# Performance work log

Measured on AMD Instinct MI355X. Metric: run time of the kernel, lower is better.

The kernel has to match this reference:

```python
import jax, jax.numpy as jnp
import numpy as np

ALPHA = 0.2  # LeakyReLU negative slope

def setup_inputs() -> dict:
    key = jax.random.key(0)
    k_h, k_adj, k_W, k_a = jax.random.split(key, 4)
    B, N, F_in, F_out = 8, 2048, 256, 64
    h = jax.random.normal(k_h, (B, N, F_in), dtype=jnp.float32)
    adj = jax.random.randint(k_adj, (B, N, N), 0, 2, dtype=jnp.int32)
    # nn.Linear weights: W [F_out, F_in], a [1, 2*F_out]
    W = jax.random.normal(k_W, (F_out, F_in), dtype=jnp.float32) * (1.0 / np.sqrt(F_in))
    a = jax.random.normal(k_a, (1, 2 * F_out), dtype=jnp.float32) * (1.0 / np.sqrt(2 * F_out))
    return {"h": h, "adj": adj, "W": W, "a": a}

def reference(h, adj, W, a):
    # Wh = h @ W^T : [B, N, F_out]
    Wh = jnp.einsum('bnf,of->bno', h, W)
    F_out = Wh.shape[-1]
    # a([Wi, Wj]) decomposes: e_ij = a_i . Wh_i + a_j . Wh_j (no O(N^2 * 2F) concat)
    a_i = a[0, :F_out]   # [F_out]
    a_j = a[0, F_out:]   # [F_out]
    e_i = Wh @ a_i       # [B, N]
    e_j = Wh @ a_j       # [B, N]
    e = jax.nn.leaky_relu(e_i[:, :, None] + e_j[:, None, :], negative_slope=ALPHA)  # [B, N, N]
    e = jnp.where(adj == 0, -jnp.inf, e)
    att = jnp.nan_to_num(jax.nn.softmax(e, axis=-1), nan=0.0)
    # dropout is identity in eval mode
    return jnp.einsum('bnm,bmo->bno', att, Wh)
```

## Files before the change

### kernel.cpp

```cpp
#include <hip/hip_runtime.h>

typedef float f32x4 __attribute__((ext_vector_type(4)));
typedef __bf16 bf16x8 __attribute__((ext_vector_type(8)));
typedef int i32x4 __attribute__((ext_vector_type(4)));
typedef unsigned short u16;
typedef unsigned int u32;

#define ALPHA 0.2f

__device__ __forceinline__ u16 f2bf(float x) {
    u32 u = __float_as_uint(x);
    u += 0x7FFFu + ((u >> 16) & 1u);
    return (u16)(u >> 16);
}

__global__ __launch_bounds__(256) void k_wh(
    const float* __restrict__ hsrc, const float* __restrict__ Wsrc,
    const float* __restrict__ asrc,
    u16* __restrict__ WhbT,
    float* __restrict__ ei, float* __restrict__ ej)
{
    __shared__ float Wl[64][68];
    __shared__ float hl[64][68];
    __shared__ __align__(16) u16 tl[4096];

    const int tid = threadIdx.x;
    const int tx = tid & 15, ty = tid >> 4;
    const int R0 = blockIdx.x * 64;

    float acc[4][4] = {};

    for (int kc = 0; kc < 4; ++kc) {
        const int k0 = kc * 64;
        __syncthreads();
        #pragma unroll
        for (int p = 0; p < 4; ++p) {
            int idx = p * 1024 + tid * 4;
            int row = idx >> 6, k = idx & 63;
            float4 wv4 = *reinterpret_cast<const float4*>(&Wsrc[row * 256 + k0 + k]);
            Wl[k + 0][row] = wv4.x; Wl[k + 1][row] = wv4.y;
            Wl[k + 2][row] = wv4.z; Wl[k + 3][row] = wv4.w;
            float4 hv4 = *reinterpret_cast<const float4*>(&hsrc[(size_t)(R0 + row) * 256 + k0 + k]);
            hl[k + 0][row] = hv4.x; hl[k + 1][row] = hv4.y;
            hl[k + 2][row] = hv4.z; hl[k + 3][row] = hv4.w;
        }
        __syncthreads();
        #pragma unroll 4
        for (int k = 0; k < 64; ++k) {
            float4 hv = *reinterpret_cast<const float4*>(&hl[k][4 * ty]);
            float4 wv = *reinterpret_cast<const float4*>(&Wl[k][4 * tx]);
            float hr[4] = {hv.x, hv.y, hv.z, hv.w};
            float wc[4] = {wv.x, wv.y, wv.z, wv.w};
            #pragma unroll
            for (int i = 0; i < 4; ++i)
                #pragma unroll
                for (int j = 0; j < 4; ++j)
                    acc[i][j] = fmaf(hr[i], wc[j], acc[i][j]);
        }
    }

    float4 av_i = *reinterpret_cast<const float4*>(&asrc[4 * tx]);
    float4 av_j = *reinterpret_cast<const float4*>(&asrc[64 + 4 * tx]);
    #pragma unroll
    for (int i = 0; i < 4; ++i) {
        float pi = acc[i][0]*av_i.x + acc[i][1]*av_i.y + acc[i][2]*av_i.z + acc[i][3]*av_i.w;
        float pj = acc[i][0]*av_j.x + acc[i][1]*av_j.y + acc[i][2]*av_j.z + acc[i][3]*av_j.w;
        #pragma unroll
        for (int off = 1; off < 16; off <<= 1) {
            pi += __shfl_xor(pi, off, 64);
            pj += __shfl_xor(pj, off, 64);
        }
        if (tx == 0) {
            ei[R0 + 4 * ty + i] = pi;
            ej[R0 + 4 * ty + i] = pj;
        }
    }

    #pragma unroll
    for (int i = 0; i < 4; ++i)
        #pragma unroll
        for (int j = 0; j < 4; ++j) {
            int row = 4 * tx + j;
            int col = 4 * ty + i;
            tl[(row * 64 + col) ^ ((row & 7) << 3)] = f2bf(acc[i][j]);
        }
    __syncthreads();
    {
        const int b = blockIdx.x >> 5;
        const int nloc = (blockIdx.x & 31) * 64;
        const int o = tid >> 2, rg = tid & 3;
        #pragma unroll
        for (int c = 0; c < 2; ++c) {
            int u = (o * 64 + rg * 16 + 8 * c) ^ ((o & 7) << 3);
            int4 v = *reinterpret_cast<const int4*>(&tl[u]);
            *reinterpret_cast<int4*>(&WhbT[(size_t)(b * 64 + o) * 2048 + nloc + rg * 16 + 8 * c]) = v;
        }
    }
}

__global__ __launch_bounds__(256) void k_attn(
    const int* __restrict__ adj, const u16* __restrict__ WhbT,
    const float* __restrict__ ei_g, const float* __restrict__ ej_g,
    float* __restrict__ out)
{
    __shared__ float accl[2][64][21];

    const int tid   = threadIdx.x;
    const int lane  = tid & 63;
    const int wid   = tid >> 6;
    const int b     = blockIdx.x >> 6;
    const int blk   = blockIdx.x & 63;
    const int strip = wid & 1;
    const int half  = wid >> 1;
    const int n0    = blk * 32 + strip * 16;
    const int r     = lane & 15;
    const int ks    = lane >> 4;

    const int*   adjp = adj  + (size_t)(b * 2048 + n0 + r) * 2048 + half * 1024 + ks * 8;
    const float* ejp  = ej_g + b * 2048 + half * 1024 + ks * 8;
    const u16*   whp  = WhbT + (size_t)(b * 64 + r) * 2048 + half * 1024 + ks * 8;

    i32x4 Aa0, Aa1, Ba0, Ba1;
    float4 Ae0, Ae1, Be0, Be1;
    bf16x8 Aw0, Aw1, Aw2, Aw3, Bw0, Bw1, Bw2, Bw3;

#define LOADS(t, a0,a1,e0,e1,w0,w1,w2,w3) { \
    const int mo_ = (t) * 32; \
    a0 = *reinterpret_cast<const i32x4*>(adjp + mo_); \
    a1 = *reinterpret_cast<const i32x4*>(adjp + mo_ + 4); \
    e0 = *reinterpret_cast<const float4*>(ejp + mo_); \
    e1 = *reinterpret_cast<const float4*>(ejp + mo_ + 4); \
    w0 = *reinterpret_cast<const bf16x8*>(whp + mo_); \
    w1 = *reinterpret_cast<const bf16x8*>(whp + 32768 + mo_); \
    w2 = *reinterpret_cast<const bf16x8*>(whp + 65536 + mo_); \
    w3 = *reinterpret_cast<const bf16x8*>(whp + 98304 + mo_); }

    LOADS(0, Aa0,Aa1,Ae0,Ae1,Aw0,Aw1,Aw2,Aw3);
    LOADS(1, Ba0,Ba1,Be0,Be1,Bw0,Bw1,Bw2,Bw3);

    float mj = -1e30f;
    #pragma unroll
    for (int i = 0; i < 8; ++i) {
        float4 v = *reinterpret_cast<const float4*>(&ej_g[b * 2048 + (i * 64 + lane) * 4]);
        mj = fmaxf(mj, fmaxf(fmaxf(v.x, v.y), fmaxf(v.z, v.w)));
    }
    #pragma unroll
    for (int off = 1; off < 64; off <<= 1) mj = fmaxf(mj, __shfl_xor(mj, off, 64));

    const float eiv = ei_g[b * 2048 + n0 + r];
    const float xM  = eiv + mj;
    const float M   = fmaxf(xM, ALPHA * xM);

    bf16x8 bones;
    {
        const float o = (r == 0) ? 1.0f : 0.0f;
        #pragma unroll
        for (int j = 0; j < 8; ++j) bones[j] = (__bf16)o;
    }

    f32x4 acc0 = {}, acc1 = {}, acc2 = {}, acc3 = {}, acc4 = {};

#define PVAL(av, ev, dst) { \
    float e_ = eiv + (ev); \
    float lr_ = fmaxf(e_, ALPHA * e_); \
    float p_ = __expf(lr_ - M); \
    dst = (__bf16)(((av) != 0) ? p_ : 0.0f); }

#define PSTEP(a0,a1,e0,e1,w0,w1,w2,w3) { \
    bf16x8 af; \
    PVAL(a0.x, e0.x, af[0]); PVAL(a0.y, e0.y, af[1]); \
    PVAL(a0.z, e0.z, af[2]); PVAL(a0.w, e0.w, af[3]); \
    PVAL(a1.x, e1.x, af[4]); PVAL(a1.y, e1.y, af[5]); \
    PVAL(a1.z, e1.z, af[6]); PVAL(a1.w, e1.w, af[7]); \
    acc0 = __builtin_amdgcn_mfma_f32_16x16x32_bf16(af, w0, acc0, 0, 0, 0); \
    acc1 = __builtin_amdgcn_mfma_f32_16x16x32_bf16(af, w1, acc1, 0, 0, 0); \
    acc2 = __builtin_amdgcn_mfma_f32_16x16x32_bf16(af, w2, acc2, 0, 0, 0); \
    acc3 = __builtin_amdgcn_mfma_f32_16x16x32_bf16(af, w3, acc3, 0, 0, 0); \
    acc4 = __builtin_amdgcn_mfma_f32_16x16x32_bf16(af, bones, acc4, 0, 0, 0); }

    for (int k = 0; k < 15; ++k) {
        const int t = 2 * k;
        PSTEP(Aa0,Aa1,Ae0,Ae1,Aw0,Aw1,Aw2,Aw3);
        LOADS(t + 2, Aa0,Aa1,Ae0,Ae1,Aw0,Aw1,Aw2,Aw3);
        PSTEP(Ba0,Ba1,Be0,Be1,Bw0,Bw1,Bw2,Bw3);
        LOADS(t + 3, Ba0,Ba1,Be0,Be1,Bw0,Bw1,Bw2,Bw3);
    }
    PSTEP(Aa0,Aa1,Ae0,Ae1,Aw0,Aw1,Aw2,Aw3);
    PSTEP(Ba0,Ba1,Be0,Be1,Bw0,Bw1,Bw2,Bw3);

#undef LOADS
#undef PSTEP
#undef PVAL

    if (half == 1) {
        #pragma unroll
        for (int q = 0; q < 4; ++q) {
            accl[strip][lane][q]      = acc0[q];
            accl[strip][lane][4 + q]  = acc1[q];
            accl[strip][lane][8 + q]  = acc2[q];
            accl[strip][lane][12 + q] = acc3[q];
            accl[strip][lane][16 + q] = acc4[q];
        }
    }
    __syncthreads();
    if (half == 0) {
        #pragma unroll
        for (int q = 0; q < 4; ++q) {
            acc0[q] += accl[strip][lane][q];
            acc1[q] += accl[strip][lane][4 + q];
            acc2[q] += accl[strip][lane][8 + q];
            acc3[q] += accl[strip][lane][12 + q];
            acc4[q] += accl[strip][lane][16 + q];
        }
        #pragma unroll
        for (int q = 0; q < 4; ++q) {
            float d   = __shfl(acc4[q], lane & 48, 64);
            float inv = (d > 0.0f) ? 1.0f / d : 0.0f;
            const int n = n0 + ks * 4 + q;
            float* op = out + (size_t)(b * 2048 + n) * 64 + r;
            op[0]  = acc0[q] * inv;
            op[16] = acc1[q] * inv;
            op[32] = acc2[q] * inv;
            op[48] = acc3[q] * inv;
        }
    }
}

extern "C" void kernel_launch(void* const* d_in, const int* in_sizes, int n_in,
                              void* d_out, int out_size, void* d_ws, size_t ws_size,
                              hipStream_t stream)
{
    const float* h   = (const float*)d_in[0];
    const int*   adj = (const int*)d_in[1];
    const float* W   = (const float*)d_in[2];
    const float* a   = (const float*)d_in[3];
    float* out = (float*)d_out;

    u16*   WhbT = (u16*)d_ws;
    float* ei   = (float*)((char*)d_ws + 2 * 1024 * 1024);
    float* ej   = ei + 16384;

    k_wh<<<dim3(256), dim3(256), 0, stream>>>(h, W, a, WhbT, ei, ej);
    k_attn<<<dim3(512), dim3(256), 0, stream>>>(adj, WhbT, ei, ej, out);
}
```

Baseline: 69.93 us.

## Pack adjacency into bitmasks in the Wh kernel and split attention over four waves

Extra blocks in the first kernel read the int32 adjacency with nontemporal loads and pack it into 32-bit bitmasks laid out for the attention kernel. The attention kernel then loads one int4 of mask bits per lane instead of streaming the full adjacency row inside the MFMA loop. The column range is now split across four waves per 16-row strip (1024 blocks), and partial sums are reduced through shared memory. The dense adjacency is still read once, so the gain depends on taking that stream out of the compute loop and overlapping it with the Wh GEMM, at the cost of an extra workspace round trip.

```diff
diff --git a/kernel.cpp b/kernel.cpp
--- a/kernel.cpp
+++ b/kernel.cpp
@@ -7,6 +7,7 @@
 typedef unsigned int u32;
 
 #define ALPHA 0.2f
+#define NPACK 2048
 
 __device__ __forceinline__ u16 f2bf(float x) {
     u32 u = __float_as_uint(x);
@@ -14,17 +15,46 @@
     return (u16)(u >> 16);
 }
 
-__global__ __launch_bounds__(256) void k_wh(
+__global__ __launch_bounds__(256) void k_wh_pack(
     const float* __restrict__ hsrc, const float* __restrict__ Wsrc,
-    const float* __restrict__ asrc,
+    const float* __restrict__ asrc, const int* __restrict__ adj,
     u16* __restrict__ WhbT,
-    float* __restrict__ ei, float* __restrict__ ej)
+    float* __restrict__ ei, float* __restrict__ ej,
+    u32* __restrict__ adjq)
 {
     __shared__ float Wl[64][68];
     __shared__ float hl[64][68];
     __shared__ __align__(16) u16 tl[4096];
 
     const int tid = threadIdx.x;
+
+    if (blockIdx.x >= 256) {
+        int i = (blockIdx.x - 256) * 256 + tid;
+        #pragma unroll
+        for (int it = 0; it < 2; ++it, i += NPACK * 256) {
+            const int T = i & 3, ks = (i >> 2) & 3, q = (i >> 4) & 3;
+            const int row = i >> 6;
+            const int* base = adj + (size_t)row * 2048 + q * 512 + ks * 8;
+            u32 bits = 0;
+            #pragma unroll
+            for (int dt = 0; dt < 4; ++dt) {
+                const int c0 = (4 * T + dt) * 32;
+                i32x4 v0 = __builtin_nontemporal_load(
+                    reinterpret_cast<const i32x4*>(base + c0));
+                i32x4 v1 = __builtin_nontemporal_load(
+                    reinterpret_cast<const i32x4*>(base + c0 + 4));
+                u32 m = 0;
+                m |= (v0[0] != 0) ? 1u : 0u;  m |= (v0[1] != 0) ? 2u : 0u;
+                m |= (v0[2] != 0) ? 4u : 0u;  m |= (v0[3] != 0) ? 8u : 0u;
+                m |= (v1[0] != 0) ? 16u : 0u; m |= (v1[1] != 0) ? 32u : 0u;
+                m |= (v1[2] != 0) ? 64u : 0u; m |= (v1[3] != 0) ? 128u : 0u;
+                bits |= m << (dt * 8);
+            }
+            adjq[i] = bits;
+        }
+        return;
+    }
+
     const int tx = tid & 15, ty = tid >> 4;
     const int R0 = blockIdx.x * 64;
 
@@ -98,36 +128,52 @@
     }
 }
 
-__global__ __launch_bounds__(256) void k_attn(
-    const int* __restrict__ adj, const u16* __restrict__ WhbT,
+__global__ __launch_bounds__(256, 4) void k_attn(
+    const u32* __restrict__ adjq, const u16* __restrict__ WhbT,
     const float* __restrict__ ei_g, const float* __restrict__ ej_g,
     float* __restrict__ out)
 {
-    __shared__ float accl[2][64][21];
-
-    const int tid   = threadIdx.x;
-    const int lane  = tid & 63;
-    const int wid   = tid >> 6;
-    const int b     = blockIdx.x >> 6;
-    const int blk   = blockIdx.x & 63;
-    const int strip = wid & 1;
-    const int half  = wid >> 1;
-    const int n0    = blk * 32 + strip * 16;
-    const int r     = lane & 15;
-    const int ks    = lane >> 4;
-
-    const int*   adjp = adj  + (size_t)(b * 2048 + n0 + r) * 2048 + half * 1024 + ks * 8;
-    const float* ejp  = ej_g + b * 2048 + half * 1024 + ks * 8;
-    const u16*   whp  = WhbT + (size_t)(b * 64 + r) * 2048 + half * 1024 + ks * 8;
-
-    i32x4 Aa0, Aa1, Ba0, Ba1;
+    __shared__ float accl[3][64][21];
+
+    const int tid  = threadIdx.x;
+    const int lane = tid & 63;
+    const int mq   = tid >> 6;
+    const int b    = blockIdx.x >> 7;
+    const int n0   = (blockIdx.x & 127) * 16;
+    const int r    = lane & 15;
+    const int ks   = lane >> 4;
+
+    const float* ejp = ej_g + b * 2048 + mq * 512 + ks * 8;
+    const u16*   whp = WhbT + (size_t)(b * 64 + r) * 2048 + mq * 512 + ks * 8;
+
+    const i32x4 W4 = *reinterpret_cast<const i32x4*>(
+        &adjq[(size_t)(((b * 2048 + n0 + r) * 4 + mq) * 4 + ks) * 4]);
+
+    float mj = -1e30f;
+    #pragma unroll
+    for (int i = 0; i < 8; ++i) {
+        float4 v = *reinterpret_cast<const float4*>(&ej_g[b * 2048 + (i * 64 + lane) * 4]);
+        mj = fmaxf(mj, fmaxf(fmaxf(v.x, v.y), fmaxf(v.z, v.w)));
+    }
+    #pragma unroll
+    for (int off = 1; off < 64; off <<= 1) mj = fmaxf(mj, __shfl_xor(mj, off, 64));
+
+    const float eiv = ei_g[b * 2048 + n0 + r];
+    const float xM  = eiv + mj;
+    const float M   = fmaxf(xM, ALPHA * xM);
+
+    bf16x8 bones;
+    {
+        const float o = (r == 0) ? 1.0f : 0.0f;
+        #pragma unroll
+        for (int j = 0; j < 8; ++j) bones[j] = (__bf16)o;
+    }
+
+    f32x4 acc0 = {}, acc1 = {}, acc2 = {}, acc3 = {}, acc4 = {};
     float4 Ae0, Ae1, Be0, Be1;
     bf16x8 Aw0, Aw1, Aw2, Aw3, Bw0, Bw1, Bw2, Bw3;
 
-#define LOADS(t, a0,a1,e0,e1,w0,w1,w2,w3) { \
-    const int mo_ = (t) * 32; \
-    a0 = *reinterpret_cast<const i32x4*>(adjp + mo_); \
-    a1 = *reinterpret_cast<const i32x4*>(adjp + mo_ + 4); \
+#define LD(t, e0,e1,w0,w1,w2,w3) { const int mo_ = (t) * 32; \
     e0 = *reinterpret_cast<const float4*>(ejp + mo_); \
     e1 = *reinterpret_cast<const float4*>(ejp + mo_ + 4); \
     w0 = *reinterpret_cast<const bf16x8*>(whp + mo_); \
@@ -135,82 +181,62 @@
     w2 = *reinterpret_cast<const bf16x8*>(whp + 65536 + mo_); \
     w3 = *reinterpret_cast<const bf16x8*>(whp + 98304 + mo_); }
 
-    LOADS(0, Aa0,Aa1,Ae0,Ae1,Aw0,Aw1,Aw2,Aw3);
-    LOADS(1, Ba0,Ba1,Be0,Be1,Bw0,Bw1,Bw2,Bw3);
-
-    float mj = -1e30f;
-    #pragma unroll
-    for (int i = 0; i < 8; ++i) {
-        float4 v = *reinterpret_cast<const float4*>(&ej_g[b * 2048 + (i * 64 + lane) * 4]);
-        mj = fmaxf(mj, fmaxf(fmaxf(v.x, v.y), fmaxf(v.z, v.w)));
-    }
-    #pragma unroll
-    for (int off = 1; off < 64; off <<= 1) mj = fmaxf(mj, __shfl_xor(mj, off, 64));
-
-    const float eiv = ei_g[b * 2048 + n0 + r];
-    const float xM  = eiv + mj;
-    const float M   = fmaxf(xM, ALPHA * xM);
-
-    bf16x8 bones;
-    {
-        const float o = (r == 0) ? 1.0f : 0.0f;
-        #pragma unroll
-        for (int j = 0; j < 8; ++j) bones[j] = (__bf16)o;
-    }
-
-    f32x4 acc0 = {}, acc1 = {}, acc2 = {}, acc3 = {}, acc4 = {};
-
-#define PVAL(av, ev, dst) { \
+#define PVAL(mk, ev, dst) { \
     float e_ = eiv + (ev); \
     float lr_ = fmaxf(e_, ALPHA * e_); \
     float p_ = __expf(lr_ - M); \
-    dst = (__bf16)(((av) != 0) ? p_ : 0.0f); }
-
-#define PSTEP(a0,a1,e0,e1,w0,w1,w2,w3) { \
+    dst = (__bf16)((mk) ? p_ : 0.0f); }
+
+#define TILE(t, e0,e1,w0,w1,w2,w3) { \
+    const u32 byv = ((u32)W4[(t) >> 2]) >> (((t) & 3) * 8); \
     bf16x8 af; \
-    PVAL(a0.x, e0.x, af[0]); PVAL(a0.y, e0.y, af[1]); \
-    PVAL(a0.z, e0.z, af[2]); PVAL(a0.w, e0.w, af[3]); \
-    PVAL(a1.x, e1.x, af[4]); PVAL(a1.y, e1.y, af[5]); \
-    PVAL(a1.z, e1.z, af[6]); PVAL(a1.w, e1.w, af[7]); \
+    PVAL(byv & 1u,   e0.x, af[0]); PVAL(byv & 2u,   e0.y, af[1]); \
+    PVAL(byv & 4u,   e0.z, af[2]); PVAL(byv & 8u,   e0.w, af[3]); \
+    PVAL(byv & 16u,  e1.x, af[4]); PVAL(byv & 32u,  e1.y, af[5]); \
+    PVAL(byv & 64u,  e1.z, af[6]); PVAL(byv & 128u, e1.w, af[7]); \
     acc0 = __builtin_amdgcn_mfma_f32_16x16x32_bf16(af, w0, acc0, 0, 0, 0); \
     acc1 = __builtin_amdgcn_mfma_f32_16x16x32_bf16(af, w1, acc1, 0, 0, 0); \
     acc2 = __builtin_amdgcn_mfma_f32_16x16x32_bf16(af, w2, acc2, 0, 0, 0); \
     acc3 = __builtin_amdgcn_mfma_f32_16x16x32_bf16(af, w3, acc3, 0, 0, 0); \
     acc4 = __builtin_amdgcn_mfma_f32_16x16x32_bf16(af, bones, acc4, 0, 0, 0); }
 
-    for (int k = 0; k < 15; ++k) {
-        const int t = 2 * k;
-        PSTEP(Aa0,Aa1,Ae0,Ae1,Aw0,Aw1,Aw2,Aw3);
-        LOADS(t + 2, Aa0,Aa1,Ae0,Ae1,Aw0,Aw1,Aw2,Aw3);
-        PSTEP(Ba0,Ba1,Be0,Be1,Bw0,Bw1,Bw2,Bw3);
-        LOADS(t + 3, Ba0,Ba1,Be0,Be1,Bw0,Bw1,Bw2,Bw3);
-    }
-    PSTEP(Aa0,Aa1,Ae0,Ae1,Aw0,Aw1,Aw2,Aw3);
-    PSTEP(Ba0,Ba1,Be0,Be1,Bw0,Bw1,Bw2,Bw3);
-
-#undef LOADS
-#undef PSTEP
+#define PAIR(t) \
+    TILE(t,   Ae0,Ae1,Aw0,Aw1,Aw2,Aw3); LD((t)+2, Ae0,Ae1,Aw0,Aw1,Aw2,Aw3); \
+    TILE((t)+1, Be0,Be1,Bw0,Bw1,Bw2,Bw3); LD((t)+3, Be0,Be1,Bw0,Bw1,Bw2,Bw3);
+
+    LD(0, Ae0,Ae1,Aw0,Aw1,Aw2,Aw3);
+    LD(1, Be0,Be1,Bw0,Bw1,Bw2,Bw3);
+    PAIR(0); PAIR(2); PAIR(4); PAIR(6); PAIR(8); PAIR(10); PAIR(12);
+    TILE(14, Ae0,Ae1,Aw0,Aw1,Aw2,Aw3);
+    TILE(15, Be0,Be1,Bw0,Bw1,Bw2,Bw3);
+
+#undef PAIR
+#undef TILE
 #undef PVAL
-
-    if (half == 1) {
+#undef LD
+
+    if (mq != 0) {
         #pragma unroll
         for (int q = 0; q < 4; ++q) {
-            accl[strip][lane][q]      = acc0[q];
-            accl[strip][lane][4 + q]  = acc1[q];
-            accl[strip][lane][8 + q]  = acc2[q];
-            accl[strip][lane][12 + q] = acc3[q];
-            accl[strip][lane][16 + q] = acc4[q];
+            accl[mq - 1][lane][q]      = acc0[q];
+            accl[mq - 1][lane][4 + q]  = acc1[q];
+            accl[mq - 1][lane][8 + q]  = acc2[q];
+            accl[mq - 1][lane][12 + q] = acc3[q];
+            accl[mq - 1][lane][16 + q] = acc4[q];
         }
     }
     __syncthreads();
-    if (half == 0) {
-        #pragma unroll
-        for (int q = 0; q < 4; ++q) {
-            acc0[q] += accl[strip][lane][q];
-            acc1[q] += accl[strip][lane][4 + q];
-            acc2[q] += accl[strip][lane][8 + q];
-            acc3[q] += accl[strip][lane][12 + q];
-            acc4[q] += accl[strip][lane][16 + q];
+    if (mq == 0) {
+        #pragma unroll
+        for (int w = 0; w < 3; ++w) {
+            #pragma unroll
+            for (int q = 0; q < 4; ++q) {
+                acc0[q] += accl[w][lane][q];
+                acc1[q] += accl[w][lane][4 + q];
+                acc2[q] += accl[w][lane][8 + q];
+                acc3[q] += accl[w][lane][12 + q];
+                acc4[q] += accl[w][lane][16 + q];
+            }
         }
         #pragma unroll
         for (int q = 0; q < 4; ++q) {
@@ -239,7 +265,8 @@
     u16*   WhbT = (u16*)d_ws;
     float* ei   = (float*)((char*)d_ws + 2 * 1024 * 1024);
     float* ej   = ei + 16384;
-
-    k_wh<<<dim3(256), dim3(256), 0, stream>>>(h, W, a, WhbT, ei, ej);
-    k_attn<<<dim3(512), dim3(256), 0, stream>>>(adj, WhbT, ei, ej, out);
-}
+    u32*   adjq = (u32*)((char*)d_ws + 3 * 1024 * 1024);
+
+    k_wh_pack<<<dim3(256 + NPACK), dim3(256), 0, stream>>>(h, W, a, adj, WhbT, ei, ej, adjq);
+    k_attn<<<dim3(1024), dim3(256), 0, stream>>>(adjq, WhbT, ei, ej, out);
+}
```

Result: slower. 71.52 us (+2.3%).

## Stage Wh tiles in LDS, widen row tiles, split-K partials with normalize kernel

Applied to the files above, without the earlier changes.

The attention kernel now has each block handle 64 rows and one half of the key dimension. The bf16 Wh^T chunk and ej values are staged in shared memory and reused by all four waves, instead of each wave streaming Wh from global memory. Adjacency rows are read with nontemporal loads, four steps deep, and block indices are remapped so blocks are interleaved across batches. Partial numerators and denominators from the two halves go to workspace, and a third kernel sums and normalizes them. This adds a launch, extra global traffic for the partials, and barriers inside the main loop.

```diff
diff --git a/kernel.cpp b/kernel.cpp
--- a/kernel.cpp
+++ b/kernel.cpp
@@ -101,42 +101,42 @@
 __global__ __launch_bounds__(256) void k_attn(
     const int* __restrict__ adj, const u16* __restrict__ WhbT,
     const float* __restrict__ ei_g, const float* __restrict__ ej_g,
-    float* __restrict__ out)
-{
-    __shared__ float accl[2][64][21];
-
-    const int tid   = threadIdx.x;
-    const int lane  = tid & 63;
-    const int wid   = tid >> 6;
-    const int b     = blockIdx.x >> 6;
-    const int blk   = blockIdx.x & 63;
-    const int strip = wid & 1;
-    const int half  = wid >> 1;
-    const int n0    = blk * 32 + strip * 16;
-    const int r     = lane & 15;
-    const int ks    = lane >> 4;
-
-    const int*   adjp = adj  + (size_t)(b * 2048 + n0 + r) * 2048 + half * 1024 + ks * 8;
-    const float* ejp  = ej_g + b * 2048 + half * 1024 + ks * 8;
-    const u16*   whp  = WhbT + (size_t)(b * 64 + r) * 2048 + half * 1024 + ks * 8;
-
-    i32x4 Aa0, Aa1, Ba0, Ba1;
-    float4 Ae0, Ae1, Be0, Be1;
-    bf16x8 Aw0, Aw1, Aw2, Aw3, Bw0, Bw1, Bw2, Bw3;
-
-#define LOADS(t, a0,a1,e0,e1,w0,w1,w2,w3) { \
-    const int mo_ = (t) * 32; \
-    a0 = *reinterpret_cast<const i32x4*>(adjp + mo_); \
-    a1 = *reinterpret_cast<const i32x4*>(adjp + mo_ + 4); \
-    e0 = *reinterpret_cast<const float4*>(ejp + mo_); \
-    e1 = *reinterpret_cast<const float4*>(ejp + mo_ + 4); \
-    w0 = *reinterpret_cast<const bf16x8*>(whp + mo_); \
-    w1 = *reinterpret_cast<const bf16x8*>(whp + 32768 + mo_); \
-    w2 = *reinterpret_cast<const bf16x8*>(whp + 65536 + mo_); \
-    w3 = *reinterpret_cast<const bf16x8*>(whp + 98304 + mo_); }
-
-    LOADS(0, Aa0,Aa1,Ae0,Ae1,Aw0,Aw1,Aw2,Aw3);
-    LOADS(1, Ba0,Ba1,Be0,Be1,Bw0,Bw1,Bw2,Bw3);
+    float* __restrict__ nump, float* __restrict__ denp)
+{
+    __shared__ __align__(16) u16 whl[64 * 264];
+    __shared__ __align__(16) float ejl[1024];
+
+    const int tid  = threadIdx.x;
+    const int lane = tid & 63;
+    const int w    = tid >> 6;
+    const int lb = (blockIdx.x & 7) * 64 + (blockIdx.x >> 3);
+    const int mt = lb & 1;
+    const int nt = (lb >> 1) & 31;
+    const int b  = lb >> 6;
+    const int r  = lane & 15;
+    const int ks = lane >> 4;
+    const int m0 = mt * 1024;
+
+    {
+        float4 v = *reinterpret_cast<const float4*>(&ej_g[b * 2048 + m0 + tid * 4]);
+        *reinterpret_cast<float4*>(&ejl[tid * 4]) = v;
+    }
+
+    const u16* whb = WhbT + (size_t)b * 131072;
+    const int sf = tid >> 2;
+    const int su = (tid & 3) * 8;
+    int4 pv0, pv1, pv2, pv3, pv4, pv5, pv6, pv7;
+#define PLOAD(p) { const u16* pp = whb + sf * 2048 + m0 + (p) * 256 + su * 8; \
+    pv0 = *reinterpret_cast<const int4*>(pp);      pv1 = *reinterpret_cast<const int4*>(pp + 8); \
+    pv2 = *reinterpret_cast<const int4*>(pp + 16); pv3 = *reinterpret_cast<const int4*>(pp + 24); \
+    pv4 = *reinterpret_cast<const int4*>(pp + 32); pv5 = *reinterpret_cast<const int4*>(pp + 40); \
+    pv6 = *reinterpret_cast<const int4*>(pp + 48); pv7 = *reinterpret_cast<const int4*>(pp + 56); }
+#define PWRITE() { char* wp = reinterpret_cast<char*>(whl) + sf * 528 + su * 16; \
+    *reinterpret_cast<int4*>(wp)       = pv0; *reinterpret_cast<int4*>(wp + 16)  = pv1; \
+    *reinterpret_cast<int4*>(wp + 32)  = pv2; *reinterpret_cast<int4*>(wp + 48)  = pv3; \
+    *reinterpret_cast<int4*>(wp + 64)  = pv4; *reinterpret_cast<int4*>(wp + 80)  = pv5; \
+    *reinterpret_cast<int4*>(wp + 96)  = pv6; *reinterpret_cast<int4*>(wp + 112) = pv7; }
+    PLOAD(0);
 
     float mj = -1e30f;
     #pragma unroll
@@ -147,7 +147,7 @@
     #pragma unroll
     for (int off = 1; off < 64; off <<= 1) mj = fmaxf(mj, __shfl_xor(mj, off, 64));
 
-    const float eiv = ei_g[b * 2048 + n0 + r];
+    const float eiv = ei_g[b * 2048 + nt * 64 + w * 16 + r];
     const float xM  = eiv + mj;
     const float M   = fmaxf(xM, ALPHA * xM);
 
@@ -158,72 +158,98 @@
         for (int j = 0; j < 8; ++j) bones[j] = (__bf16)o;
     }
 
+    const int* adjp = adj + (size_t)(b * 2048 + nt * 64 + w * 16 + r) * 2048 + m0 + ks * 8;
+
+    i32x4 Aa0, Aa1, Ba0, Ba1, Ca0, Ca1, Da0, Da1;
+#define LADJ(gt, x0, x1) if ((gt) < 32) { \
+    x0 = __builtin_nontemporal_load(reinterpret_cast<const i32x4*>(adjp + (gt) * 32)); \
+    x1 = __builtin_nontemporal_load(reinterpret_cast<const i32x4*>(adjp + (gt) * 32 + 4)); }
+    LADJ(0, Aa0, Aa1); LADJ(1, Ba0, Ba1); LADJ(2, Ca0, Ca1); LADJ(3, Da0, Da1);
+
+    PWRITE();
+    __syncthreads();
+
     f32x4 acc0 = {}, acc1 = {}, acc2 = {}, acc3 = {}, acc4 = {};
 
-#define PVAL(av, ev, dst) { \
+    const char* wl0 = reinterpret_cast<const char*>(whl) + r * 528 + ks * 16;
+    const float* eb = ejl + ks * 8;
+
+#define PVAL(mk, ev, dst) { \
     float e_ = eiv + (ev); \
     float lr_ = fmaxf(e_, ALPHA * e_); \
     float p_ = __expf(lr_ - M); \
-    dst = (__bf16)(((av) != 0) ? p_ : 0.0f); }
-
-#define PSTEP(a0,a1,e0,e1,w0,w1,w2,w3) { \
+    dst = (__bf16)(((mk) != 0) ? p_ : 0.0f); }
+
+#define STEP(gt, x0, x1) { \
+    const int tl_ = (gt) & 7; \
+    float4 e0 = *reinterpret_cast<const float4*>(eb + (gt) * 32); \
+    float4 e1 = *reinterpret_cast<const float4*>(eb + (gt) * 32 + 4); \
     bf16x8 af; \
-    PVAL(a0.x, e0.x, af[0]); PVAL(a0.y, e0.y, af[1]); \
-    PVAL(a0.z, e0.z, af[2]); PVAL(a0.w, e0.w, af[3]); \
-    PVAL(a1.x, e1.x, af[4]); PVAL(a1.y, e1.y, af[5]); \
-    PVAL(a1.z, e1.z, af[6]); PVAL(a1.w, e1.w, af[7]); \
+    PVAL(x0[0], e0.x, af[0]); PVAL(x0[1], e0.y, af[1]); \
+    PVAL(x0[2], e0.z, af[2]); PVAL(x0[3], e0.w, af[3]); \
+    PVAL(x1[0], e1.x, af[4]); PVAL(x1[1], e1.y, af[5]); \
+    PVAL(x1[2], e1.z, af[6]); PVAL(x1[3], e1.w, af[7]); \
+    bf16x8 w0 = *reinterpret_cast<const bf16x8*>(wl0 + tl_ * 64); \
+    bf16x8 w1 = *reinterpret_cast<const bf16x8*>(wl0 + tl_ * 64 + 16 * 528); \
+    bf16x8 w2 = *reinterpret_cast<const bf16x8*>(wl0 + tl_ * 64 + 32 * 528); \
+    bf16x8 w3 = *reinterpret_cast<const bf16x8*>(wl0 + tl_ * 64 + 48 * 528); \
     acc0 = __builtin_amdgcn_mfma_f32_16x16x32_bf16(af, w0, acc0, 0, 0, 0); \
     acc1 = __builtin_amdgcn_mfma_f32_16x16x32_bf16(af, w1, acc1, 0, 0, 0); \
     acc2 = __builtin_amdgcn_mfma_f32_16x16x32_bf16(af, w2, acc2, 0, 0, 0); \
     acc3 = __builtin_amdgcn_mfma_f32_16x16x32_bf16(af, w3, acc3, 0, 0, 0); \
     acc4 = __builtin_amdgcn_mfma_f32_16x16x32_bf16(af, bones, acc4, 0, 0, 0); }
 
-    for (int k = 0; k < 15; ++k) {
-        const int t = 2 * k;
-        PSTEP(Aa0,Aa1,Ae0,Ae1,Aw0,Aw1,Aw2,Aw3);
-        LOADS(t + 2, Aa0,Aa1,Ae0,Ae1,Aw0,Aw1,Aw2,Aw3);
-        PSTEP(Ba0,Ba1,Be0,Be1,Bw0,Bw1,Bw2,Bw3);
-        LOADS(t + 3, Ba0,Ba1,Be0,Be1,Bw0,Bw1,Bw2,Bw3);
-    }
-    PSTEP(Aa0,Aa1,Ae0,Ae1,Aw0,Aw1,Aw2,Aw3);
-    PSTEP(Ba0,Ba1,Be0,Be1,Bw0,Bw1,Bw2,Bw3);
-
-#undef LOADS
-#undef PSTEP
+    #pragma unroll
+    for (int p = 0; p < 4; ++p) {
+        if (p < 3) PLOAD(p + 1);
+        STEP(p * 8 + 0, Aa0, Aa1); LADJ(p * 8 + 4,  Aa0, Aa1);
+        STEP(p * 8 + 1, Ba0, Ba1); LADJ(p * 8 + 5,  Ba0, Ba1);
+        STEP(p * 8 + 2, Ca0, Ca1); LADJ(p * 8 + 6,  Ca0, Ca1);
+        STEP(p * 8 + 3, Da0, Da1); LADJ(p * 8 + 7,  Da0, Da1);
+        STEP(p * 8 + 4, Aa0, Aa1); LADJ(p * 8 + 8,  Aa0, Aa1);
+        STEP(p * 8 + 5, Ba0, Ba1); LADJ(p * 8 + 9,  Ba0, Ba1);
+        STEP(p * 8 + 6, Ca0, Ca1); LADJ(p * 8 + 10, Ca0, Ca1);
+        STEP(p * 8 + 7, Da0, Da1); LADJ(p * 8 + 11, Da0, Da1);
+        if (p < 3) {
+            __syncthreads();
+            PWRITE();
+            __syncthreads();
+        }
+    }
+#undef STEP
 #undef PVAL
-
-    if (half == 1) {
-        #pragma unroll
-        for (int q = 0; q < 4; ++q) {
-            accl[strip][lane][q]      = acc0[q];
-            accl[strip][lane][4 + q]  = acc1[q];
-            accl[strip][lane][8 + q]  = acc2[q];
-            accl[strip][lane][12 + q] = acc3[q];
-            accl[strip][lane][16 + q] = acc4[q];
-        }
-    }
-    __syncthreads();
-    if (half == 0) {
-        #pragma unroll
-        for (int q = 0; q < 4; ++q) {
-            acc0[q] += accl[strip][lane][q];
-            acc1[q] += accl[strip][lane][4 + q];
-            acc2[q] += accl[strip][lane][8 + q];
-            acc3[q] += accl[strip][lane][12 + q];
-            acc4[q] += accl[strip][lane][16 + q];
-        }
-        #pragma unroll
-        for (int q = 0; q < 4; ++q) {
-            float d   = __shfl(acc4[q], lane & 48, 64);
-            float inv = (d > 0.0f) ? 1.0f / d : 0.0f;
-            const int n = n0 + ks * 4 + q;
-            float* op = out + (size_t)(b * 2048 + n) * 64 + r;
-            op[0]  = acc0[q] * inv;
-            op[16] = acc1[q] * inv;
-            op[32] = acc2[q] * inv;
-            op[48] = acc3[q] * inv;
-        }
-    }
+#undef LADJ
+#undef PWRITE
+#undef PLOAD
+
+    const size_t nb0 = (size_t)mt * 16384 + b * 2048 + nt * 64 + w * 16;
+    #pragma unroll
+    for (int q = 0; q < 4; ++q) {
+        const int rr = ks * 4 + q;
+        float* np = nump + (nb0 + rr) * 64 + r;
+        np[0]  = acc0[q];
+        np[16] = acc1[q];
+        np[32] = acc2[q];
+        np[48] = acc3[q];
+        if (r == 0) denp[nb0 + rr] = acc4[q];
+    }
+}
+
+__global__ __launch_bounds__(256) void k_norm(
+    const float* __restrict__ nump, const float* __restrict__ denp,
+    float* __restrict__ out)
+{
+    const int tid = threadIdx.x;
+    const int f4 = tid & 15;
+    const size_t N = (size_t)blockIdx.x * 16 + (tid >> 4);
+    const float d = denp[N] + denp[16384 + N];
+    const float inv = (d > 0.0f) ? 1.0f / d : 0.0f;
+    float4 a = *reinterpret_cast<const float4*>(&nump[N * 64 + f4 * 4]);
+    float4 c = *reinterpret_cast<const float4*>(&nump[(16384 + N) * 64 + f4 * 4]);
+    float4 o;
+    o.x = (a.x + c.x) * inv; o.y = (a.y + c.y) * inv;
+    o.z = (a.z + c.z) * inv; o.w = (a.w + c.w) * inv;
+    *reinterpret_cast<float4*>(&out[N * 64 + f4 * 4]) = o;
 }
 
 extern "C" void kernel_launch(void* const* d_in, const int* in_sizes, int n_in,
@@ -239,7 +265,10 @@
     u16*   WhbT = (u16*)d_ws;
     float* ei   = (float*)((char*)d_ws + 2 * 1024 * 1024);
     float* ej   = ei + 16384;
-
-    k_wh<<<dim3(256), dim3(256), 0, stream>>>(h, W, a, WhbT, ei, ej);
-    k_attn<<<dim3(512), dim3(256), 0, stream>>>(adj, WhbT, ei, ej, out);
-}
+    float* nump = (float*)((char*)d_ws + 4 * 1024 * 1024);
+    float* denp = (float*)((char*)d_ws + 12 * 1024 * 1024);
+
+    k_wh  <<<dim3(256),  dim3(256), 0, stream>>>(h, W, a, WhbT, ei, ej);
+    k_attn<<<dim3(512),  dim3(256), 0, stream>>>(adj, WhbT, ei, ej, nump, denp);
+    k_norm<<<dim3(1024), dim3(256), 0, stream>>>(nump, denp, out);
+}
```

Result: faster. 64.91 us (-7.2%).

## Prefetch whole adjacency slice into bitmasks and split attention K four ways

Applied to the files above, without the earlier changes.

Each wave now issues all sixteen of its adjacency vector loads up front as nontemporal loads and packs them into 32-bit masks. This puts many more bytes in flight for the bandwidth-bound int32 adjacency stream. Blocks now cover 16 rows with four waves each owning a quarter of the columns, and partial results are combined through shared memory. The grid doubles to 1024 blocks and is remapped so the eight consecutive block IDs go to different batches. The ej values are staged in LDS pre-scaled by log2(e), so the softmax numerator can use exp2f. The cost is higher register pressure from the 32 live adjacency vectors, which the launch bound of 4 blocks per CU may force into spills, plus a larger cross-wave reduction.

```diff
diff --git a/kernel.cpp b/kernel.cpp
--- a/kernel.cpp
+++ b/kernel.cpp
@@ -7,6 +7,7 @@
 typedef unsigned int u32;
 
 #define ALPHA 0.2f
+#define LOG2E 1.4426950408889634f
 
 __device__ __forceinline__ u16 f2bf(float x) {
     u32 u = __float_as_uint(x);
@@ -98,45 +99,22 @@
     }
 }
 
-__global__ __launch_bounds__(256) void k_attn(
+__global__ __launch_bounds__(256, 4) void k_attn(
     const int* __restrict__ adj, const u16* __restrict__ WhbT,
     const float* __restrict__ ei_g, const float* __restrict__ ej_g,
     float* __restrict__ out)
 {
-    __shared__ float accl[2][64][21];
-
-    const int tid   = threadIdx.x;
-    const int lane  = tid & 63;
-    const int wid   = tid >> 6;
-    const int b     = blockIdx.x >> 6;
-    const int blk   = blockIdx.x & 63;
-    const int strip = wid & 1;
-    const int half  = wid >> 1;
-    const int n0    = blk * 32 + strip * 16;
-    const int r     = lane & 15;
-    const int ks    = lane >> 4;
-
-    const int*   adjp = adj  + (size_t)(b * 2048 + n0 + r) * 2048 + half * 1024 + ks * 8;
-    const float* ejp  = ej_g + b * 2048 + half * 1024 + ks * 8;
-    const u16*   whp  = WhbT + (size_t)(b * 64 + r) * 2048 + half * 1024 + ks * 8;
-
-    i32x4 Aa0, Aa1, Ba0, Ba1;
-    float4 Ae0, Ae1, Be0, Be1;
-    bf16x8 Aw0, Aw1, Aw2, Aw3, Bw0, Bw1, Bw2, Bw3;
-
-#define LOADS(t, a0,a1,e0,e1,w0,w1,w2,w3) { \
-    const int mo_ = (t) * 32; \
-    a0 = *reinterpret_cast<const i32x4*>(adjp + mo_); \
-    a1 = *reinterpret_cast<const i32x4*>(adjp + mo_ + 4); \
-    e0 = *reinterpret_cast<const float4*>(ejp + mo_); \
-    e1 = *reinterpret_cast<const float4*>(ejp + mo_ + 4); \
-    w0 = *reinterpret_cast<const bf16x8*>(whp + mo_); \
-    w1 = *reinterpret_cast<const bf16x8*>(whp + 32768 + mo_); \
-    w2 = *reinterpret_cast<const bf16x8*>(whp + 65536 + mo_); \
-    w3 = *reinterpret_cast<const bf16x8*>(whp + 98304 + mo_); }
-
-    LOADS(0, Aa0,Aa1,Ae0,Ae1,Aw0,Aw1,Aw2,Aw3);
-    LOADS(1, Ba0,Ba1,Be0,Be1,Bw0,Bw1,Bw2,Bw3);
+    __shared__ float ejl[4][520];
+    __shared__ float comb[3][64][21];
+
+    const int tid  = threadIdx.x;
+    const int lane = tid & 63;
+    const int mq   = tid >> 6;
+    const int lb   = (int)(blockIdx.x & 7) * 128 + (int)(blockIdx.x >> 3);
+    const int b    = lb >> 7;
+    const int n0   = (lb & 127) * 16;
+    const int r    = lane & 15;
+    const int ks   = lane >> 4;
 
     float mj = -1e30f;
     #pragma unroll
@@ -147,9 +125,55 @@
     #pragma unroll
     for (int off = 1; off < 64; off <<= 1) mj = fmaxf(mj, __shfl_xor(mj, off, 64));
 
-    const float eiv = ei_g[b * 2048 + n0 + r];
-    const float xM  = eiv + mj;
-    const float M   = fmaxf(xM, ALPHA * xM);
+    const float eiv2 = ei_g[b * 2048 + n0 + r] * LOG2E;
+    const float xM2  = eiv2 + mj * LOG2E;
+    const float M2   = fmaxf(xM2, ALPHA * xM2);
+
+    {
+        float4 v0 = *reinterpret_cast<const float4*>(&ej_g[b * 2048 + mq * 512 + lane * 8]);
+        float4 v1 = *reinterpret_cast<const float4*>(&ej_g[b * 2048 + mq * 512 + lane * 8 + 4]);
+        v0.x *= LOG2E; v0.y *= LOG2E; v0.z *= LOG2E; v0.w *= LOG2E;
+        v1.x *= LOG2E; v1.y *= LOG2E; v1.z *= LOG2E; v1.w *= LOG2E;
+        *reinterpret_cast<float4*>(&ejl[mq][lane * 8])     = v0;
+        *reinterpret_cast<float4*>(&ejl[mq][lane * 8 + 4]) = v1;
+    }
+
+    const int* adjp = adj + (size_t)(b * 2048 + n0 + r) * 2048 + mq * 512 + ks * 8;
+    u32 bits0 = 0, bits1 = 0, bits2 = 0, bits3 = 0;
+    i32x4 Aq0, Aq1, Bq0, Bq1, Cq0, Cq1, Dq0, Dq1;
+    i32x4 Eq0, Eq1, Fq0, Fq1, Gq0, Gq1, Hq0, Hq1;
+
+#define LA(t, x0, x1) { \
+    x0 = __builtin_nontemporal_load(reinterpret_cast<const i32x4*>(adjp + (t) * 32)); \
+    x1 = __builtin_nontemporal_load(reinterpret_cast<const i32x4*>(adjp + (t) * 32 + 4)); }
+#define PK(x0, x1, W, sh) { u32 m_ = 0; \
+    m_ |= (x0[0] != 0) ? 1u   : 0u; m_ |= (x0[1] != 0) ? 2u   : 0u; \
+    m_ |= (x0[2] != 0) ? 4u   : 0u; m_ |= (x0[3] != 0) ? 8u   : 0u; \
+    m_ |= (x1[0] != 0) ? 16u  : 0u; m_ |= (x1[1] != 0) ? 32u  : 0u; \
+    m_ |= (x1[2] != 0) ? 64u  : 0u; m_ |= (x1[3] != 0) ? 128u : 0u; \
+    W |= m_ << (sh); }
+
+    LA(0, Aq0, Aq1); LA(1, Bq0, Bq1); LA(2, Cq0, Cq1); LA(3, Dq0, Dq1);
+    LA(4, Eq0, Eq1); LA(5, Fq0, Fq1); LA(6, Gq0, Gq1); LA(7, Hq0, Hq1);
+
+    PK(Aq0, Aq1, bits0, 0);  LA(8,  Aq0, Aq1);
+    PK(Bq0, Bq1, bits0, 8);  LA(9,  Bq0, Bq1);
+    PK(Cq0, Cq1, bits0, 16); LA(10, Cq0, Cq1);
+    PK(Dq0, Dq1, bits0, 24); LA(11, Dq0, Dq1);
+    PK(Eq0, Eq1, bits1, 0);  LA(12, Eq0, Eq1);
+    PK(Fq0, Fq1, bits1, 8);  LA(13, Fq0, Fq1);
+    PK(Gq0, Gq1, bits1, 16); LA(14, Gq0, Gq1);
+    PK(Hq0, Hq1, bits1, 24); LA(15, Hq0, Hq1);
+    PK(Aq0, Aq1, bits2, 0);
+    PK(Bq0, Bq1, bits2, 8);
+    PK(Cq0, Cq1, bits2, 16);
+    PK(Dq0, Dq1, bits2, 24);
+    PK(Eq0, Eq1, bits3, 0);
+    PK(Fq0, Fq1, bits3, 8);
+    PK(Gq0, Gq1, bits3, 16);
+    PK(Hq0, Hq1, bits3, 24);
+#undef PK
+#undef LA
 
     bf16x8 bones;
     {
@@ -158,59 +182,83 @@
         for (int j = 0; j < 8; ++j) bones[j] = (__bf16)o;
     }
 
+    const u16*   whp = WhbT + (size_t)(b * 64 + r) * 2048 + mq * 512 + ks * 8;
+    const float* eb  = &ejl[mq][ks * 8];
+
+    bf16x8 Aw0, Aw1, Aw2, Aw3, Bw0, Bw1, Bw2, Bw3;
+#define LDW(t, w0, w1, w2, w3) { const u16* pp = whp + (t) * 32; \
+    w0 = *reinterpret_cast<const bf16x8*>(pp); \
+    w1 = *reinterpret_cast<const bf16x8*>(pp + 32768); \
+    w2 = *reinterpret_cast<const bf16x8*>(pp + 65536); \
+    w3 = *reinterpret_cast<const bf16x8*>(pp + 98304); }
+
+#define PVAL(mk, ev, dst) { \
+    float x_ = eiv2 + (ev); \
+    float lr_ = fmaxf(x_, ALPHA * x_); \
+    float p_ = exp2f(lr_ - M2); \
+    dst = (__bf16)(((mk) != 0u) ? p_ : 0.0f); }
+
     f32x4 acc0 = {}, acc1 = {}, acc2 = {}, acc3 = {}, acc4 = {};
 
-#define PVAL(av, ev, dst) { \
-    float e_ = eiv + (ev); \
-    float lr_ = fmaxf(e_, ALPHA * e_); \
-    float p_ = __expf(lr_ - M); \
-    dst = (__bf16)(((av) != 0) ? p_ : 0.0f); }
-
-#define PSTEP(a0,a1,e0,e1,w0,w1,w2,w3) { \
+#define STEP(t, BW, w0, w1, w2, w3) { \
+    const u32 by_ = (BW) >> (((t) & 3) * 8); \
+    float4 e0 = *reinterpret_cast<const float4*>(eb + (t) * 32); \
+    float4 e1 = *reinterpret_cast<const float4*>(eb + (t) * 32 + 4); \
     bf16x8 af; \
-    PVAL(a0.x, e0.x, af[0]); PVAL(a0.y, e0.y, af[1]); \
-    PVAL(a0.z, e0.z, af[2]); PVAL(a0.w, e0.w, af[3]); \
-    PVAL(a1.x, e1.x, af[4]); PVAL(a1.y, e1.y, af[5]); \
-    PVAL(a1.z, e1.z, af[6]); PVAL(a1.w, e1.w, af[7]); \
+    PVAL(by_ & 1u,   e0.x, af[0]); PVAL(by_ & 2u,   e0.y, af[1]); \
+    PVAL(by_ & 4u,   e0.z, af[2]); PVAL(by_ & 8u,   e0.w, af[3]); \
+    PVAL(by_ & 16u,  e1.x, af[4]); PVAL(by_ & 32u,  e1.y, af[5]); \
+    PVAL(by_ & 64u,  e1.z, af[6]); PVAL(by_ & 128u, e1.w, af[7]); \
     acc0 = __builtin_amdgcn_mfma_f32_16x16x32_bf16(af, w0, acc0, 0, 0, 0); \
     acc1 = __builtin_amdgcn_mfma_f32_16x16x32_bf16(af, w1, acc1, 0, 0, 0); \
     acc2 = __builtin_amdgcn_mfma_f32_16x16x32_bf16(af, w2, acc2, 0, 0, 0); \
     acc3 = __builtin_amdgcn_mfma_f32_16x16x32_bf16(af, w3, acc3, 0, 0, 0); \
     acc4 = __builtin_amdgcn_mfma_f32_16x16x32_bf16(af, bones, acc4, 0, 0, 0); }
 
-    for (int k = 0; k < 15; ++k) {
-        const int t = 2 * k;
-        PSTEP(Aa0,Aa1,Ae0,Ae1,Aw0,Aw1,Aw2,Aw3);
-        LOADS(t + 2, Aa0,Aa1,Ae0,Ae1,Aw0,Aw1,Aw2,Aw3);
-        PSTEP(Ba0,Ba1,Be0,Be1,Bw0,Bw1,Bw2,Bw3);
-        LOADS(t + 3, Ba0,Ba1,Be0,Be1,Bw0,Bw1,Bw2,Bw3);
-    }
-    PSTEP(Aa0,Aa1,Ae0,Ae1,Aw0,Aw1,Aw2,Aw3);
-    PSTEP(Ba0,Ba1,Be0,Be1,Bw0,Bw1,Bw2,Bw3);
-
-#undef LOADS
-#undef PSTEP
+    LDW(0, Aw0, Aw1, Aw2, Aw3);
+    LDW(1, Bw0, Bw1, Bw2, Bw3);
+    STEP(0,  bits0, Aw0, Aw1, Aw2, Aw3); LDW(2,  Aw0, Aw1, Aw2, Aw3);
+    STEP(1,  bits0, Bw0, Bw1, Bw2, Bw3); LDW(3,  Bw0, Bw1, Bw2, Bw3);
+    STEP(2,  bits0, Aw0, Aw1, Aw2, Aw3); LDW(4,  Aw0, Aw1, Aw2, Aw3);
+    STEP(3,  bits0, Bw0, Bw1, Bw2, Bw3); LDW(5,  Bw0, Bw1, Bw2, Bw3);
+    STEP(4,  bits1, Aw0, Aw1, Aw2, Aw3); LDW(6,  Aw0, Aw1, Aw2, Aw3);
+    STEP(5,  bits1, Bw0, Bw1, Bw2, Bw3); LDW(7,  Bw0, Bw1, Bw2, Bw3);
+    STEP(6,  bits1, Aw0, Aw1, Aw2, Aw3); LDW(8,  Aw0, Aw1, Aw2, Aw3);
+    STEP(7,  bits1, Bw0, Bw1, Bw2, Bw3); LDW(9,  Bw0, Bw1, Bw2, Bw3);
+    STEP(8,  bits2, Aw0, Aw1, Aw2, Aw3); LDW(10, Aw0, Aw1, Aw2, Aw3);
+    STEP(9,  bits2, Bw0, Bw1, Bw2, Bw3); LDW(11, Bw0, Bw1, Bw2, Bw3);
+    STEP(10, bits2, Aw0, Aw1, Aw2, Aw3); LDW(12, Aw0, Aw1, Aw2, Aw3);
+    STEP(11, bits2, Bw0, Bw1, Bw2, Bw3); LDW(13, Bw0, Bw1, Bw2, Bw3);
+    STEP(12, bits3, Aw0, Aw1, Aw2, Aw3); LDW(14, Aw0, Aw1, Aw2, Aw3);
+    STEP(13, bits3, Bw0, Bw1, Bw2, Bw3); LDW(15, Bw0, Bw1, Bw2, Bw3);
+    STEP(14, bits3, Aw0, Aw1, Aw2, Aw3);
+    STEP(15, bits3, Bw0, Bw1, Bw2, Bw3);
+#undef STEP
 #undef PVAL
-
-    if (half == 1) {
+#undef LDW
+
+    if (mq != 0) {
         #pragma unroll
         for (int q = 0; q < 4; ++q) {
-            accl[strip][lane][q]      = acc0[q];
-            accl[strip][lane][4 + q]  = acc1[q];
-            accl[strip][lane][8 + q]  = acc2[q];
-            accl[strip][lane][12 + q] = acc3[q];
-            accl[strip][lane][16 + q] = acc4[q];
+            comb[mq - 1][lane][q]      = acc0[q];
+            comb[mq - 1][lane][4 + q]  = acc1[q];
+            comb[mq - 1][lane][8 + q]  = acc2[q];
+            comb[mq - 1][lane][12 + q] = acc3[q];
+            comb[mq - 1][lane][16 + q] = acc4[q];
         }
     }
     __syncthreads();
-    if (half == 0) {
-        #pragma unroll
-        for (int q = 0; q < 4; ++q) {
-            acc0[q] += accl[strip][lane][q];
-            acc1[q] += accl[strip][lane][4 + q];
-            acc2[q] += accl[strip][lane][8 + q];
-            acc3[q] += accl[strip][lane][12 + q];
-            acc4[q] += accl[strip][lane][16 + q];
+    if (mq == 0) {
+        #pragma unroll
+        for (int w = 0; w < 3; ++w) {
+            #pragma unroll
+            for (int q = 0; q < 4; ++q) {
+                acc0[q] += comb[w][lane][q];
+                acc1[q] += comb[w][lane][4 + q];
+                acc2[q] += comb[w][lane][8 + q];
+                acc3[q] += comb[w][lane][12 + q];
+                acc4[q] += comb[w][lane][16 + q];
+            }
         }
         #pragma unroll
         for (int q = 0; q < 4; ++q) {
@@ -240,6 +288,6 @@
     float* ei   = (float*)((char*)d_ws + 2 * 1024 * 1024);
     float* ej   = ei + 16384;
 
-    k_wh<<<dim3(256), dim3(256), 0, stream>>>(h, W, a, WhbT, ei, ej);
-    k_attn<<<dim3(512), dim3(256), 0, stream>>>(adj, WhbT, ei, ej, out);
-}
+    k_wh  <<<dim3(256),  dim3(256), 0, stream>>>(h, W, a, WhbT, ei, ej);
+    k_attn<<<dim3(1024), dim3(256), 0, stream>>>(adj, WhbT, ei, ej, out);
+}
```

New measurement: 84.24 us. 1.2x slower.
